# Kernel tuning notes

Measured on AMD Instinct MI355X. Metric: run time of the kernel, lower is better.

The kernel has to match this reference:

```python
import jax, jax.numpy as jnp
import numpy as np

N = 200000      # n_edges (1-simplices)
NNZ = 2000000   # nonzeros per sparse Laplacian
F_IN = 64       # num_edge_feats
F_H = 32        # f_size (hard-coded in FlowSAN)
F_OUT = 8       # output_size
G = 256         # number of graphs in batch
NEG_SLOPE = 0.2 # GAT LeakyReLU slope


def setup_inputs() -> dict:
    key = jax.random.key(0)
    ks = iter(jax.random.split(key, 64))

    def rn(shape, s=0.1):
        return jax.random.normal(next(ks), shape, dtype=jnp.float32) * s

    d = {"x1": jax.random.normal(next(ks), (N, F_IN), dtype=jnp.float32)}
    dims = [(F_IN, F_H), (F_H, F_H), (F_H, F_H), (F_H, F_OUT)]
    for i, (fi, fo) in enumerate(dims, 1):
        d[f"pW{i}"] = rn((fi, fo))                      # SANLayer.p_layer weight (bias=False)
        d[f"uW{i}"] = rn((fi, fo))                      # l_u GAT linear
        d[f"ua_s{i}"] = rn((fo,)); d[f"ua_d{i}"] = rn((fo,))  # l_u GAT attention vec halves
        d[f"dW{i}"] = rn((fi, fo))                      # l_d GAT linear
        d[f"da_s{i}"] = rn((fo,)); d[f"da_d{i}"] = rn((fo,))
    d["l1_idx"] = jax.random.randint(next(ks), (2, NNZ), 0, N, dtype=jnp.int32)
    d["l1_val"] = jax.random.normal(next(ks), (NNZ,), dtype=jnp.float32)
    d["lu_idx"] = jax.random.randint(next(ks), (2, NNZ), 0, N, dtype=jnp.int32)
    d["ld_idx"] = jax.random.randint(next(ks), (2, NNZ), 0, N, dtype=jnp.int32)
    d["batch1"] = jnp.sort(jax.random.randint(next(ks), (N,), 0, G, dtype=jnp.int32))
    return d


def _gat(x, W, a_s, a_d, idx):
    # GAT-style attention over the nonzero pattern of the sparse Laplacian
    h = x @ W                                   # [N, fo]
    row, col = idx[0], idx[1]
    e = jax.nn.leaky_relu(h[row] @ a_s + h[col] @ a_d, NEG_SLOPE)  # [nnz]
    e = e - jax.ops.segment_max(e, row, num_segments=N)[row]       # stable softmax
    w = jnp.exp(e)
    alpha = w / (jax.ops.segment_sum(w, row, num_segments=N)[row] + 1e-16)
    return jax.ops.segment_sum(alpha[:, None] * h[col], row, num_segments=N)


def _san(x, pW, uW, ua_s, ua_d, dW, da_s, da_d, l1_idx, l1_val, lu_idx, ld_idx):
    # p branch: torch.sparse.mm(L1, x @ pW)
    hp = x @ pW
    row, col = l1_idx[0], l1_idx[1]
    hp = jax.ops.segment_sum(l1_val[:, None] * hp[col], row, num_segments=N)
    hu = _gat(x, uW, ua_s, ua_d, lu_idx)
    hd = _gat(x, dW, da_s, da_d, ld_idx)
    return hu + hd + hp


def reference(x1,
              pW1, uW1, ua_s1, ua_d1, dW1, da_s1, da_d1,
              pW2, uW2, ua_s2, ua_d2, dW2, da_s2, da_d2,
              pW3, uW3, ua_s3, ua_d3, dW3, da_s3, da_d3,
              pW4, uW4, ua_s4, ua_d4, dW4, da_s4, da_d4,
              l1_idx, l1_val, lu_idx, ld_idx, batch1):
    layers = [
        (pW1, uW1, ua_s1, ua_d1, dW1, da_s1, da_d1),
        (pW2, uW2, ua_s2, ua_d2, dW2, da_s2, da_d2),
        (pW3, uW3, ua_s3, ua_d3, dW3, da_s3, da_d3),
        (pW4, uW4, ua_s4, ua_d4, dW4, da_s4, da_d4),
    ]
    x = x1
    for p in layers:
        x = jax.nn.relu(_san(x, *p, l1_idx, l1_val, lu_idx, ld_idx))
    # global_mean_pool(|x|, batch1)
    cnt = jax.ops.segment_sum(jnp.ones((N,), jnp.float32), batch1, num_segments=G)
    pooled = jax.ops.segment_sum(jnp.abs(x), batch1, num_segments=G) / jnp.maximum(cnt, 1.0)[:, None]
    return jax.nn.softmax(pooled, axis=1)
```

## Files before the change

### kernel.cpp

```cpp
#include <hip/hip_runtime.h>
#include <cmath>


#define N_    200000
#define NNZ_  2000000
#define G_    256


__global__ __launch_bounds__(256) void hist_k(const int* __restrict__ lu, const int* __restrict__ ld,
                                              const int* __restrict__ l1, int* __restrict__ deg,
                                              int* __restrict__ tick) {
    int i = blockIdx.x * 256 + threadIdx.x;
    if (i >= NNZ_ / 4) return;
    int e = i * 4;
    int4 ru = *reinterpret_cast<const int4*>(lu + e);
    int4 rd = *reinterpret_cast<const int4*>(ld + e);
    int4 rl = *reinterpret_cast<const int4*>(l1 + e);
    int4 t;
    t.x = atomicAdd(&deg[ru.x], 1);
    t.y = atomicAdd(&deg[ru.y], 1);
    t.z = atomicAdd(&deg[ru.z], 1);
    t.w = atomicAdd(&deg[ru.w], 1);
    *reinterpret_cast<int4*>(tick + e) = t;
    t.x = atomicAdd(&deg[N_ + rd.x], 1);
    t.y = atomicAdd(&deg[N_ + rd.y], 1);
    t.z = atomicAdd(&deg[N_ + rd.z], 1);
    t.w = atomicAdd(&deg[N_ + rd.w], 1);
    *reinterpret_cast<int4*>(tick + NNZ_ + e) = t;
    t.x = atomicAdd(&deg[2 * N_ + rl.x], 1);
    t.y = atomicAdd(&deg[2 * N_ + rl.y], 1);
    t.z = atomicAdd(&deg[2 * N_ + rl.z], 1);
    t.w = atomicAdd(&deg[2 * N_ + rl.w], 1);
    *reinterpret_cast<int4*>(tick + 2 * NNZ_ + e) = t;
}

__global__ __launch_bounds__(256) void scan1_k(const int* __restrict__ in, int* __restrict__ out,
                                               int* __restrict__ bsum, int n) {
    __shared__ int lds[256];
    int tid = threadIdx.x;
    int base = blockIdx.x * 1024 + tid * 4;
    int v0 = (base + 0 < n) ? in[base + 0] : 0;
    int v1 = (base + 1 < n) ? in[base + 1] : 0;
    int v2 = (base + 2 < n) ? in[base + 2] : 0;
    int v3 = (base + 3 < n) ? in[base + 3] : 0;
    int s = v0 + v1 + v2 + v3;
    lds[tid] = s;
    __syncthreads();
    for (int off = 1; off < 256; off <<= 1) {
        int t = (tid >= off) ? lds[tid - off] : 0;
        __syncthreads();
        lds[tid] += t;
        __syncthreads();
    }
    int excl = lds[tid] - s;
    if (base + 0 < n) out[base + 0] = excl;
    if (base + 1 < n) out[base + 1] = excl + v0;
    if (base + 2 < n) out[base + 2] = excl + v0 + v1;
    if (base + 3 < n) out[base + 3] = excl + v0 + v1 + v2;
    if (tid == 255) bsum[blockIdx.x] = lds[255];
}

__global__ __launch_bounds__(256) void scan2_k(int* __restrict__ bsum, int nb, int* __restrict__ total_out) {
    __shared__ int lds[256];
    __shared__ int run_s;
    int tid = threadIdx.x;
    if (tid == 0) run_s = 0;
    __syncthreads();
    for (int c0 = 0; c0 < nb; c0 += 256) {
        int i = c0 + tid;
        int s = (i < nb) ? bsum[i] : 0;
        lds[tid] = s;
        __syncthreads();
        for (int off = 1; off < 256; off <<= 1) {
            int t = (tid >= off) ? lds[tid - off] : 0;
            __syncthreads();
            lds[tid] += t;
            __syncthreads();
        }
        int run = run_s;
        if (i < nb) bsum[i] = run + lds[tid] - s;
        __syncthreads();
        if (tid == 0) run_s = run + lds[255];
        __syncthreads();
    }
    if (tid == 0 && total_out) *total_out = run_s;
}

__global__ __launch_bounds__(256) void scan3_k(int* __restrict__ out, const int* __restrict__ bsum, int n) {
    int add = bsum[blockIdx.x];
    int base = blockIdx.x * 1024 + threadIdx.x * 4;
    #pragma unroll
    for (int k = 0; k < 4; ++k)
        if (base + k < n) out[base + k] += add;
}


template <int FI, int FO, int SCB>
__global__ __launch_bounds__(256) void scat_gemm_k(
    const int* __restrict__ lu, const int* __restrict__ ld, const int* __restrict__ l1,
    const float* __restrict__ l1v, const int* __restrict__ rptr, const int* __restrict__ tick,
    int* __restrict__ cols, float* __restrict__ vcsr,
    const float* __restrict__ x,
    const float* __restrict__ uW, const float* __restrict__ uas, const float* __restrict__ uad,
    const float* __restrict__ dW, const float* __restrict__ das, const float* __restrict__ dad,
    const float* __restrict__ pW,
    float* __restrict__ HU, float* __restrict__ HD, float* __restrict__ HP,
    float* __restrict__ ssu, float* __restrict__ sdu,
    float* __restrict__ ssd, float* __restrict__ sdd) {
    if (blockIdx.x < SCB) {
        int i = blockIdx.x * 256 + threadIdx.x;
        if (i >= NNZ_ / 4) return;
        int e = i * 4;
        int4 ru = *reinterpret_cast<const int4*>(lu + e);
        int4 rd = *reinterpret_cast<const int4*>(ld + e);
        int4 rl = *reinterpret_cast<const int4*>(l1 + e);
        int4 cu = *reinterpret_cast<const int4*>(lu + NNZ_ + e);
        int4 cd = *reinterpret_cast<const int4*>(ld + NNZ_ + e);
        int4 cl = *reinterpret_cast<const int4*>(l1 + NNZ_ + e);
        int4 tu = *reinterpret_cast<const int4*>(tick + e);
        int4 td = *reinterpret_cast<const int4*>(tick + NNZ_ + e);
        int4 tl = *reinterpret_cast<const int4*>(tick + 2 * NNZ_ + e);
        float4 v = *reinterpret_cast<const float4*>(l1v + e);
        int pu0 = rptr[ru.x] + tu.x, pu1 = rptr[ru.y] + tu.y;
        int pu2 = rptr[ru.z] + tu.z, pu3 = rptr[ru.w] + tu.w;
        int pd0 = rptr[N_ + rd.x] + td.x, pd1 = rptr[N_ + rd.y] + td.y;
        int pd2 = rptr[N_ + rd.z] + td.z, pd3 = rptr[N_ + rd.w] + td.w;
        int pl0 = rptr[2 * N_ + rl.x] + tl.x, pl1 = rptr[2 * N_ + rl.y] + tl.y;
        int pl2 = rptr[2 * N_ + rl.z] + tl.z, pl3 = rptr[2 * N_ + rl.w] + tl.w;
        __builtin_nontemporal_store(cu.x, &cols[pu0]);
        __builtin_nontemporal_store(cu.y, &cols[pu1]);
        __builtin_nontemporal_store(cu.z, &cols[pu2]);
        __builtin_nontemporal_store(cu.w, &cols[pu3]);
        __builtin_nontemporal_store(cd.x, &cols[pd0]);
        __builtin_nontemporal_store(cd.y, &cols[pd1]);
        __builtin_nontemporal_store(cd.z, &cols[pd2]);
        __builtin_nontemporal_store(cd.w, &cols[pd3]);
        __builtin_nontemporal_store(cl.x, &cols[pl0]);
        __builtin_nontemporal_store(cl.y, &cols[pl1]);
        __builtin_nontemporal_store(cl.z, &cols[pl2]);
        __builtin_nontemporal_store(cl.w, &cols[pl3]);
        __builtin_nontemporal_store(v.x, &vcsr[pl0 - 2 * NNZ_]);
        __builtin_nontemporal_store(v.y, &vcsr[pl1 - 2 * NNZ_]);
        __builtin_nontemporal_store(v.z, &vcsr[pl2 - 2 * NNZ_]);
        __builtin_nontemporal_store(v.w, &vcsr[pl3 - 2 * NNZ_]);
        return;
    }
    int bid = blockIdx.x - SCB;
    constexpr int ROWS = 256 / FO;
    constexpr int XS = FI + 1;
    __shared__ float Wu[FI * FO], Wd[FI * FO], Wp[FI * FO];
    __shared__ float xs[ROWS * XS];
    int tid = threadIdx.x;
    for (int i = tid; i < FI * FO; i += 256) {
        Wu[i] = uW[i];
        Wd[i] = dW[i];
        Wp[i] = pW[i];
    }
    int row0 = bid * ROWS;
    for (int i = tid; i < ROWS * FI; i += 256) {
        int r = i / FI, k = i - r * FI;
        int gr = row0 + r;
        xs[r * XS + k] = (gr < N_) ? x[(size_t)gr * FI + k] : 0.f;
    }
    __syncthreads();
    int r = tid / FO, j = tid - (tid / FO) * FO;
    int grow = row0 + r;
    float au = 0.f, ad = 0.f, ap = 0.f;
    #pragma unroll
    for (int k = 0; k < FI; ++k) {
        float xv = xs[r * XS + k];
        au = fmaf(xv, Wu[k * FO + j], au);
        ad = fmaf(xv, Wd[k * FO + j], ad);
        ap = fmaf(xv, Wp[k * FO + j], ap);
    }
    if (grow < N_) {
        HU[(size_t)grow * FO + j] = au;
        HD[(size_t)grow * FO + j] = ad;
        HP[(size_t)grow * FO + j] = ap;
    }
    float vsu = au * uas[j], vdu = au * uad[j];
    float vsd = ad * das[j], vdd = ad * dad[j];
    #pragma unroll
    for (int m = FO / 2; m >= 1; m >>= 1) {
        vsu += __shfl_xor(vsu, m, FO);
        vdu += __shfl_xor(vdu, m, FO);
        vsd += __shfl_xor(vsd, m, FO);
        vdd += __shfl_xor(vdd, m, FO);
    }
    if (j == 0 && grow < N_) {
        ssu[grow] = vsu; sdu[grow] = vdu;
        ssd[grow] = vsd; sdd[grow] = vdd;
    }
}


template <int FI, int FO>
__global__ __launch_bounds__(256) void gemm3_k(const float* __restrict__ x,
                                               const float* __restrict__ uW, const float* __restrict__ uas,
                                               const float* __restrict__ uad,
                                               const float* __restrict__ dW, const float* __restrict__ das,
                                               const float* __restrict__ dad,
                                               const float* __restrict__ pW,
                                               float* __restrict__ HU, float* __restrict__ HD,
                                               float* __restrict__ HP,
                                               float* __restrict__ ssu, float* __restrict__ sdu,
                                               float* __restrict__ ssd, float* __restrict__ sdd) {
    constexpr int ROWS = 256 / FO;
    constexpr int XS = FI + 1;
    __shared__ float Wu[FI * FO], Wd[FI * FO], Wp[FI * FO];
    __shared__ float xs[ROWS * XS];
    int tid = threadIdx.x;
    for (int i = tid; i < FI * FO; i += 256) {
        Wu[i] = uW[i];
        Wd[i] = dW[i];
        Wp[i] = pW[i];
    }
    int row0 = blockIdx.x * ROWS;
    for (int i = tid; i < ROWS * FI; i += 256) {
        int r = i / FI, k = i - r * FI;
        int gr = row0 + r;
        xs[r * XS + k] = (gr < N_) ? x[(size_t)gr * FI + k] : 0.f;
    }
    __syncthreads();
    int r = tid / FO, j = tid - (tid / FO) * FO;
    int grow = row0 + r;
    float au = 0.f, ad = 0.f, ap = 0.f;
    #pragma unroll
    for (int k = 0; k < FI; ++k) {
        float xv = xs[r * XS + k];
        au = fmaf(xv, Wu[k * FO + j], au);
        ad = fmaf(xv, Wd[k * FO + j], ad);
        ap = fmaf(xv, Wp[k * FO + j], ap);
    }
    if (grow < N_) {
        HU[(size_t)grow * FO + j] = au;
        HD[(size_t)grow * FO + j] = ad;
        HP[(size_t)grow * FO + j] = ap;
    }
    float vsu = au * uas[j], vdu = au * uad[j];
    float vsd = ad * das[j], vdd = ad * dad[j];
    #pragma unroll
    for (int m = FO / 2; m >= 1; m >>= 1) {
        vsu += __shfl_xor(vsu, m, FO);
        vdu += __shfl_xor(vdu, m, FO);
        vsd += __shfl_xor(vsd, m, FO);
        vdd += __shfl_xor(vdd, m, FO);
    }
    if (j == 0 && grow < N_) {
        ssu[grow] = vsu; sdu[grow] = vdu;
        ssd[grow] = vsd; sdd[grow] = vdd;
    }
}


template <int FO, bool GAT>
__device__ __forceinline__ void edge_loop(const int* __restrict__ cols, const float* __restrict__ sdv,
                                          const float* __restrict__ vals, const float* __restrict__ H,
                                          int b, int e, int lane, float s_row, int vbase,
                                          float& ax, float& ay, float& az, float& aw, float& z) {
    for (int p = b; p < e; p += 4) {
        int q1 = p + 1 < e ? p + 1 : e - 1;
        int q2 = p + 2 < e ? p + 2 : e - 1;
        int q3 = p + 3 < e ? p + 3 : e - 1;
        int c0 = cols[p], c1 = cols[q1], c2 = cols[q2], c3 = cols[q3];
        const float4 h0 = *reinterpret_cast<const float4*>(H + (size_t)c0 * FO + lane * 4);
        const float4 h1 = *reinterpret_cast<const float4*>(H + (size_t)c1 * FO + lane * 4);
        const float4 h2 = *reinterpret_cast<const float4*>(H + (size_t)c2 * FO + lane * 4);
        const float4 h3 = *reinterpret_cast<const float4*>(H + (size_t)c3 * FO + lane * 4);
        float w0, w1, w2, w3;
        if constexpr (GAT) {
            float g0 = s_row + sdv[c0];
            float g1 = s_row + sdv[c1];
            float g2 = s_row + sdv[c2];
            float g3 = s_row + sdv[c3];
            g0 = g0 > 0.f ? g0 : 0.2f * g0;
            g1 = g1 > 0.f ? g1 : 0.2f * g1;
            g2 = g2 > 0.f ? g2 : 0.2f * g2;
            g3 = g3 > 0.f ? g3 : 0.2f * g3;
            w0 = __expf(g0);
            w1 = p + 1 < e ? __expf(g1) : 0.f;
            w2 = p + 2 < e ? __expf(g2) : 0.f;
            w3 = p + 3 < e ? __expf(g3) : 0.f;
            z += (w0 + w1) + (w2 + w3);
        } else {
            w0 = vals[p - vbase];
            w1 = p + 1 < e ? vals[q1 - vbase] : 0.f;
            w2 = p + 2 < e ? vals[q2 - vbase] : 0.f;
            w3 = p + 3 < e ? vals[q3 - vbase] : 0.f;
        }
        ax = fmaf(w0, h0.x, ax); ay = fmaf(w0, h0.y, ay);
        az = fmaf(w0, h0.z, az); aw = fmaf(w0, h0.w, aw);
        ax = fmaf(w1, h1.x, ax); ay = fmaf(w1, h1.y, ay);
        az = fmaf(w1, h1.z, az); aw = fmaf(w1, h1.w, aw);
        ax = fmaf(w2, h2.x, ax); ay = fmaf(w2, h2.y, ay);
        az = fmaf(w2, h2.z, az); aw = fmaf(w2, h2.w, aw);
        ax = fmaf(w3, h3.x, ax); ay = fmaf(w3, h3.y, ay);
        az = fmaf(w3, h3.z, az); aw = fmaf(w3, h3.w, aw);
    }
}

template <int FO, int TEAMS>
__global__ __launch_bounds__(256) void gather3_k(const int* __restrict__ rptr, const int* __restrict__ cols,
                                                 const float* __restrict__ vcsr,
                                                 const float* __restrict__ HU, const float* __restrict__ HD,
                                                 const float* __restrict__ HP,
                                                 const float* __restrict__ ssu, const float* __restrict__ sdu,
                                                 const float* __restrict__ ssd, const float* __restrict__ sdd,
                                                 float* __restrict__ xout) {
    constexpr int LPR = FO / 4;
    constexpr int TPR = LPR * TEAMS;
    constexpr int RPB = 256 / TPR;
    int tid = threadIdx.x;
    int lane = tid & (LPR - 1);
    int team = (tid / LPR) & (TEAMS - 1);
    int r = blockIdx.x * RPB + tid / TPR;
    if (r >= N_) return;
    float ox = 0.f, oy = 0.f, oz = 0.f, ow = 0.f;

    auto branch = [&](const float* H, const float* sdv, const float* vals, int base, int vbase,
                      bool gat, float s_row, float& bx, float& by, float& bz, float& bw, float& z) {
        int b0 = rptr[base + r], e0 = rptr[base + r + 1];
        int half = (e0 - b0) >> 1;
        int tb = team == 0 ? b0 : b0 + half;
        int te = team == 0 ? b0 + half : e0;
        if (tb < te) {
            if (gat)
                edge_loop<FO, true>(cols, sdv, nullptr, H, tb, te, lane, s_row, 0, bx, by, bz, bw, z);
            else
                edge_loop<FO, false>(cols, nullptr, vals, H, tb, te, lane, 0.f, vbase, bx, by, bz, bw, z);
        }
        bx += __shfl_xor(bx, LPR, TPR);
        by += __shfl_xor(by, LPR, TPR);
        bz += __shfl_xor(bz, LPR, TPR);
        bw += __shfl_xor(bw, LPR, TPR);
        if (gat) z += __shfl_xor(z, LPR, TPR);
    };

    {
        float ax = 0.f, ay = 0.f, az = 0.f, aw = 0.f, z = 0.f;
        branch(HU, sdu, nullptr, 0, 0, true, ssu[r], ax, ay, az, aw, z);
        float inv = 1.f / (z + 1e-16f);
        ox = ax * inv; oy = ay * inv; oz = az * inv; ow = aw * inv;
    }
    {
        float ax = 0.f, ay = 0.f, az = 0.f, aw = 0.f, z = 0.f;
        branch(HD, sdd, nullptr, N_, 0, true, ssd[r], ax, ay, az, aw, z);
        float inv = 1.f / (z + 1e-16f);
        ox = fmaf(ax, inv, ox); oy = fmaf(ay, inv, oy);
        oz = fmaf(az, inv, oz); ow = fmaf(aw, inv, ow);
    }
    {
        float ax = 0.f, ay = 0.f, az = 0.f, aw = 0.f, z = 0.f;
        branch(HP, nullptr, vcsr, 2 * N_, 2 * NNZ_, false, 0.f, ax, ay, az, aw, z);
        ox += ax; oy += ay; oz += az; ow += aw;
    }
    if (team == 0) {
        ox = fmaxf(ox, 0.f); oy = fmaxf(oy, 0.f);
        oz = fmaxf(oz, 0.f); ow = fmaxf(ow, 0.f);
        *reinterpret_cast<float4*>(xout + (size_t)r * FO + lane * 4) = make_float4(ox, oy, oz, ow);
    }
}


__global__ __launch_bounds__(256) void pool_k(const float* __restrict__ x, const int* __restrict__ batch,
                                              float* __restrict__ out) {
    int g = blockIdx.x;
    __shared__ float part[256];
    __shared__ int sse[2];
    if (threadIdx.x < 2) {
        int target = g + threadIdx.x;
        int lo = 0, hi = N_;
        while (lo < hi) {
            int mid = (lo + hi) >> 1;
            if (batch[mid] < target) lo = mid + 1; else hi = mid;
        }
        sse[threadIdx.x] = lo;
    }
    __syncthreads();
    int s = sse[0], e = sse[1];
    int f = threadIdx.x % 8;
    float acc = 0.f;
    for (int i = s + threadIdx.x / 8; i < e; i += 32) acc += fabsf(x[(size_t)i * 8 + f]);
    part[threadIdx.x] = acc;
    __syncthreads();
    if (threadIdx.x < 8) {
        float t = 0.f;
        #pragma unroll
        for (int k = 0; k < 32; ++k) t += part[k * 8 + f];
        float cnt = (float)(e - s);
        part[f] = t / fmaxf(cnt, 1.0f);
    }
    __syncthreads();
    if (threadIdx.x == 0) {
        float m = part[0];
        for (int j = 1; j < 8; ++j) m = fmaxf(m, part[j]);
        float zs = 0.f;
        float ex[8];
        for (int j = 0; j < 8; ++j) { ex[j] = __expf(part[j] - m); zs += ex[j]; }
        for (int j = 0; j < 8; ++j) out[g * 8 + j] = ex[j] / zs;
    }
}


template <int FI, int FO>
static void run_layer(const float* xin, float* xout, const float* const* W,
                      float* HU, float* HD, float* HP,
                      float* SSU, float* SDU, float* SSD, float* SDD,
                      const int* PTR, const int* COLS, const float* VCSR, hipStream_t stream) {
    constexpr int ROWS = 256 / FO;
    constexpr int RPB = 256 / ((FO / 4) * 2);
    gemm3_k<FI, FO><<<(N_ + ROWS - 1) / ROWS, 256, 0, stream>>>(
        xin, W[1], W[2], W[3], W[4], W[5], W[6], W[0],
        HU, HD, HP, SSU, SDU, SSD, SDD);
    gather3_k<FO, 2><<<(N_ + RPB - 1) / RPB, 256, 0, stream>>>(
        PTR, COLS, VCSR, HU, HD, HP, SSU, SDU, SSD, SDD, xout);
}

extern "C" void kernel_launch(void* const* d_in, const int* in_sizes, int n_in, void* d_out,
                              int out_size, void* d_ws, size_t ws_size, hipStream_t stream) {
    (void)in_sizes; (void)n_in; (void)out_size; (void)ws_size;
    const float* x1     = (const float*)d_in[0];
    const int*   l1_idx = (const int*)d_in[29];
    const float* l1_val = (const float*)d_in[30];
    const int*   lu_idx = (const int*)d_in[31];
    const int*   ld_idx = (const int*)d_in[32];
    const int*   batch1 = (const int*)d_in[33];
    float* out = (float*)d_out;

    char* w = (char*)d_ws;
    size_t off = 0;
    auto alloc = [&](size_t bytes) -> char* {
        char* p = w + off;
        off = (off + bytes + 255) & ~(size_t)255;
        return p;
    };
    float* X    = (float*)alloc((size_t)N_ * 32 * 4);
    float* HU   = (float*)alloc((size_t)N_ * 32 * 4);
    float* HD   = (float*)alloc((size_t)N_ * 32 * 4);
    float* HP   = (float*)alloc((size_t)N_ * 32 * 4);
    float* SSU  = (float*)alloc((size_t)N_ * 4);
    float* SDU  = (float*)alloc((size_t)N_ * 4);
    float* SSD  = (float*)alloc((size_t)N_ * 4);
    float* SDD  = (float*)alloc((size_t)N_ * 4);
    int*   PTR  = (int*)alloc((size_t)(3 * N_ + 1) * 4);
    int*   DEG  = (int*)alloc((size_t)3 * N_ * 4);
    int*   BSUM = (int*)alloc((size_t)1024 * 4);
    int*   TICK = (int*)alloc((size_t)3 * NNZ_ * 4);
    int*   COLS = (int*)alloc((size_t)3 * NNZ_ * 4);
    float* VCSR = (float*)alloc((size_t)NNZ_ * 4);

    const float* W0[7] = {(const float*)d_in[1], (const float*)d_in[2], (const float*)d_in[3],
                          (const float*)d_in[4], (const float*)d_in[5], (const float*)d_in[6],
                          (const float*)d_in[7]};
    const float* W1[7] = {(const float*)d_in[8],  (const float*)d_in[9],  (const float*)d_in[10],
                          (const float*)d_in[11], (const float*)d_in[12], (const float*)d_in[13],
                          (const float*)d_in[14]};
    const float* W2[7] = {(const float*)d_in[15], (const float*)d_in[16], (const float*)d_in[17],
                          (const float*)d_in[18], (const float*)d_in[19], (const float*)d_in[20],
                          (const float*)d_in[21]};
    const float* W3[7] = {(const float*)d_in[22], (const float*)d_in[23], (const float*)d_in[24],
                          (const float*)d_in[25], (const float*)d_in[26], (const float*)d_in[27],
                          (const float*)d_in[28]};

    hipMemsetAsync(DEG, 0, (size_t)3 * N_ * 4, stream);
    constexpr int QBL = (NNZ_ / 4 + 255) / 256;
    hist_k<<<QBL, 256, 0, stream>>>(lu_idx, ld_idx, l1_idx, DEG, TICK);
    int n3 = 3 * N_;
    int nb = (n3 + 1023) / 1024;
    scan1_k<<<nb, 256, 0, stream>>>(DEG, PTR, BSUM, n3);
    scan2_k<<<1, 256, 0, stream>>>(BSUM, nb, PTR + n3);
    scan3_k<<<nb, 256, 0, stream>>>(PTR, BSUM, n3);

    {
        constexpr int ROWS = 256 / 32;
        int gemmb = (N_ + ROWS - 1) / ROWS;
        scat_gemm_k<64, 32, QBL><<<QBL + gemmb, 256, 0, stream>>>(
            lu_idx, ld_idx, l1_idx, l1_val, PTR, TICK, COLS, VCSR,
            x1, W0[1], W0[2], W0[3], W0[4], W0[5], W0[6], W0[0],
            HU, HD, HP, SSU, SDU, SSD, SDD);
    }
    {
        constexpr int RPB = 256 / ((32 / 4) * 2);
        gather3_k<32, 2><<<(N_ + RPB - 1) / RPB, 256, 0, stream>>>(
            PTR, COLS, VCSR, HU, HD, HP, SSU, SDU, SSD, SDD, X);
    }

    run_layer<32, 32>(X, X, W1, HU, HD, HP, SSU, SDU, SSD, SDD, PTR, COLS, VCSR, stream);
    run_layer<32, 32>(X, X, W2, HU, HD, HP, SSU, SDU, SSD, SDD, PTR, COLS, VCSR, stream);
    run_layer<32, 8>(X, X, W3, HU, HD, HP, SSU, SDU, SSD, SDD, PTR, COLS, VCSR, stream);

    pool_k<<<G_, 256, 0, stream>>>(X, batch1, out);
}
```

Measured before the change: 1.544 ms.

## Store projected features in fp16, pack L1 col/val, wave-per-row gather

The per-layer projections HU/HD/HP are now stored as fp16, which halves the bytes fetched by the random neighbour gathers. The L1 column index and value are packed into one int2 per edge, and the u/d column arrays are split into separate buffers. The gather kernel is rewritten to give each row one 64-lane wave: groups of lanes take different edges and each lane reads 8 half features, followed by shuffle reductions. The CSR scatter blocks are interleaved with the first-layer GEMM blocks (every 13th block) so the two kinds of work overlap. The trade-off is reduced precision of the intermediate features and wasted lanes on rows with few edges.

```diff
diff --git a/kernel.cpp b/kernel.cpp
--- a/kernel.cpp
+++ b/kernel.cpp
@@ -1,4 +1,5 @@
 #include <hip/hip_runtime.h>
+#include <hip/hip_fp16.h>
 #include <cmath>
 
 
@@ -99,16 +100,18 @@
 __global__ __launch_bounds__(256) void scat_gemm_k(
     const int* __restrict__ lu, const int* __restrict__ ld, const int* __restrict__ l1,
     const float* __restrict__ l1v, const int* __restrict__ rptr, const int* __restrict__ tick,
-    int* __restrict__ cols, float* __restrict__ vcsr,
+    int* __restrict__ cols_u, int* __restrict__ cols_d, int2* __restrict__ pl,
     const float* __restrict__ x,
     const float* __restrict__ uW, const float* __restrict__ uas, const float* __restrict__ uad,
     const float* __restrict__ dW, const float* __restrict__ das, const float* __restrict__ dad,
     const float* __restrict__ pW,
-    float* __restrict__ HU, float* __restrict__ HD, float* __restrict__ HP,
+    __half* __restrict__ HU, __half* __restrict__ HD, __half* __restrict__ HP,
     float* __restrict__ ssu, float* __restrict__ sdu,
     float* __restrict__ ssd, float* __restrict__ sdd) {
-    if (blockIdx.x < SCB) {
-        int i = blockIdx.x * 256 + threadIdx.x;
+    if (blockIdx.x % 13 == 0) {
+        int sid = blockIdx.x / 13;
+        if (sid >= SCB) return;
+        int i = sid * 256 + threadIdx.x;
         if (i >= NNZ_ / 4) return;
         int e = i * 4;
         int4 ru = *reinterpret_cast<const int4*>(lu + e);
@@ -123,29 +126,29 @@
         float4 v = *reinterpret_cast<const float4*>(l1v + e);
         int pu0 = rptr[ru.x] + tu.x, pu1 = rptr[ru.y] + tu.y;
         int pu2 = rptr[ru.z] + tu.z, pu3 = rptr[ru.w] + tu.w;
-        int pd0 = rptr[N_ + rd.x] + td.x, pd1 = rptr[N_ + rd.y] + td.y;
-        int pd2 = rptr[N_ + rd.z] + td.z, pd3 = rptr[N_ + rd.w] + td.w;
-        int pl0 = rptr[2 * N_ + rl.x] + tl.x, pl1 = rptr[2 * N_ + rl.y] + tl.y;
-        int pl2 = rptr[2 * N_ + rl.z] + tl.z, pl3 = rptr[2 * N_ + rl.w] + tl.w;
-        __builtin_nontemporal_store(cu.x, &cols[pu0]);
-        __builtin_nontemporal_store(cu.y, &cols[pu1]);
-        __builtin_nontemporal_store(cu.z, &cols[pu2]);
-        __builtin_nontemporal_store(cu.w, &cols[pu3]);
-        __builtin_nontemporal_store(cd.x, &cols[pd0]);
-        __builtin_nontemporal_store(cd.y, &cols[pd1]);
-        __builtin_nontemporal_store(cd.z, &cols[pd2]);
-        __builtin_nontemporal_store(cd.w, &cols[pd3]);
-        __builtin_nontemporal_store(cl.x, &cols[pl0]);
-        __builtin_nontemporal_store(cl.y, &cols[pl1]);
-        __builtin_nontemporal_store(cl.z, &cols[pl2]);
-        __builtin_nontemporal_store(cl.w, &cols[pl3]);
-        __builtin_nontemporal_store(v.x, &vcsr[pl0 - 2 * NNZ_]);
-        __builtin_nontemporal_store(v.y, &vcsr[pl1 - 2 * NNZ_]);
-        __builtin_nontemporal_store(v.z, &vcsr[pl2 - 2 * NNZ_]);
-        __builtin_nontemporal_store(v.w, &vcsr[pl3 - 2 * NNZ_]);
+        int pd0 = rptr[N_ + rd.x] + td.x - NNZ_, pd1 = rptr[N_ + rd.y] + td.y - NNZ_;
+        int pd2 = rptr[N_ + rd.z] + td.z - NNZ_, pd3 = rptr[N_ + rd.w] + td.w - NNZ_;
+        int pl0 = rptr[2 * N_ + rl.x] + tl.x - 2 * NNZ_, pl1 = rptr[2 * N_ + rl.y] + tl.y - 2 * NNZ_;
+        int pl2 = rptr[2 * N_ + rl.z] + tl.z - 2 * NNZ_, pl3 = rptr[2 * N_ + rl.w] + tl.w - 2 * NNZ_;
+        __builtin_nontemporal_store(cu.x, &cols_u[pu0]);
+        __builtin_nontemporal_store(cu.y, &cols_u[pu1]);
+        __builtin_nontemporal_store(cu.z, &cols_u[pu2]);
+        __builtin_nontemporal_store(cu.w, &cols_u[pu3]);
+        __builtin_nontemporal_store(cd.x, &cols_d[pd0]);
+        __builtin_nontemporal_store(cd.y, &cols_d[pd1]);
+        __builtin_nontemporal_store(cd.z, &cols_d[pd2]);
+        __builtin_nontemporal_store(cd.w, &cols_d[pd3]);
+        long long q0 = ((long long)__float_as_int(v.x) << 32) | (unsigned)cl.x;
+        long long q1 = ((long long)__float_as_int(v.y) << 32) | (unsigned)cl.y;
+        long long q2 = ((long long)__float_as_int(v.z) << 32) | (unsigned)cl.z;
+        long long q3 = ((long long)__float_as_int(v.w) << 32) | (unsigned)cl.w;
+        __builtin_nontemporal_store(q0, (long long*)&pl[pl0]);
+        __builtin_nontemporal_store(q1, (long long*)&pl[pl1]);
+        __builtin_nontemporal_store(q2, (long long*)&pl[pl2]);
+        __builtin_nontemporal_store(q3, (long long*)&pl[pl3]);
         return;
     }
-    int bid = blockIdx.x - SCB;
+    int gid = blockIdx.x - blockIdx.x / 13 - 1;
     constexpr int ROWS = 256 / FO;
     constexpr int XS = FI + 1;
     __shared__ float Wu[FI * FO], Wd[FI * FO], Wp[FI * FO];
@@ -156,7 +159,7 @@
         Wd[i] = dW[i];
         Wp[i] = pW[i];
     }
-    int row0 = bid * ROWS;
+    int row0 = gid * ROWS;
     for (int i = tid; i < ROWS * FI; i += 256) {
         int r = i / FI, k = i - r * FI;
         int gr = row0 + r;
@@ -174,9 +177,9 @@
         ap = fmaf(xv, Wp[k * FO + j], ap);
     }
     if (grow < N_) {
-        HU[(size_t)grow * FO + j] = au;
-        HD[(size_t)grow * FO + j] = ad;
-        HP[(size_t)grow * FO + j] = ap;
+        HU[(size_t)grow * FO + j] = __float2half(au);
+        HD[(size_t)grow * FO + j] = __float2half(ad);
+        HP[(size_t)grow * FO + j] = __float2half(ap);
     }
     float vsu = au * uas[j], vdu = au * uad[j];
     float vsd = ad * das[j], vdd = ad * dad[j];
@@ -201,8 +204,8 @@
                                                const float* __restrict__ dW, const float* __restrict__ das,
                                                const float* __restrict__ dad,
                                                const float* __restrict__ pW,
-                                               float* __restrict__ HU, float* __restrict__ HD,
-                                               float* __restrict__ HP,
+                                               __half* __restrict__ HU, __half* __restrict__ HD,
+                                               __half* __restrict__ HP,
                                                float* __restrict__ ssu, float* __restrict__ sdu,
                                                float* __restrict__ ssd, float* __restrict__ sdd) {
     constexpr int ROWS = 256 / FO;
@@ -233,9 +236,9 @@
         ap = fmaf(xv, Wp[k * FO + j], ap);
     }
     if (grow < N_) {
-        HU[(size_t)grow * FO + j] = au;
-        HD[(size_t)grow * FO + j] = ad;
-        HP[(size_t)grow * FO + j] = ap;
+        HU[(size_t)grow * FO + j] = __float2half(au);
+        HD[(size_t)grow * FO + j] = __float2half(ad);
+        HP[(size_t)grow * FO + j] = __float2half(ap);
     }
     float vsu = au * uas[j], vdu = au * uad[j];
     float vsd = ad * das[j], vdd = ad * dad[j];
@@ -253,111 +256,102 @@
 }
 
 
-template <int FO, bool GAT>
-__device__ __forceinline__ void edge_loop(const int* __restrict__ cols, const float* __restrict__ sdv,
-                                          const float* __restrict__ vals, const float* __restrict__ H,
-                                          int b, int e, int lane, float s_row, int vbase,
-                                          float& ax, float& ay, float& az, float& aw, float& z) {
-    for (int p = b; p < e; p += 4) {
-        int q1 = p + 1 < e ? p + 1 : e - 1;
-        int q2 = p + 2 < e ? p + 2 : e - 1;
-        int q3 = p + 3 < e ? p + 3 : e - 1;
-        int c0 = cols[p], c1 = cols[q1], c2 = cols[q2], c3 = cols[q3];
-        const float4 h0 = *reinterpret_cast<const float4*>(H + (size_t)c0 * FO + lane * 4);
-        const float4 h1 = *reinterpret_cast<const float4*>(H + (size_t)c1 * FO + lane * 4);
-        const float4 h2 = *reinterpret_cast<const float4*>(H + (size_t)c2 * FO + lane * 4);
-        const float4 h3 = *reinterpret_cast<const float4*>(H + (size_t)c3 * FO + lane * 4);
-        float w0, w1, w2, w3;
-        if constexpr (GAT) {
-            float g0 = s_row + sdv[c0];
-            float g1 = s_row + sdv[c1];
-            float g2 = s_row + sdv[c2];
-            float g3 = s_row + sdv[c3];
-            g0 = g0 > 0.f ? g0 : 0.2f * g0;
-            g1 = g1 > 0.f ? g1 : 0.2f * g1;
-            g2 = g2 > 0.f ? g2 : 0.2f * g2;
-            g3 = g3 > 0.f ? g3 : 0.2f * g3;
-            w0 = __expf(g0);
-            w1 = p + 1 < e ? __expf(g1) : 0.f;
-            w2 = p + 2 < e ? __expf(g2) : 0.f;
-            w3 = p + 3 < e ? __expf(g3) : 0.f;
-            z += (w0 + w1) + (w2 + w3);
-        } else {
-            w0 = vals[p - vbase];
-            w1 = p + 1 < e ? vals[q1 - vbase] : 0.f;
-            w2 = p + 2 < e ? vals[q2 - vbase] : 0.f;
-            w3 = p + 3 < e ? vals[q3 - vbase] : 0.f;
-        }
-        ax = fmaf(w0, h0.x, ax); ay = fmaf(w0, h0.y, ay);
-        az = fmaf(w0, h0.z, az); aw = fmaf(w0, h0.w, aw);
-        ax = fmaf(w1, h1.x, ax); ay = fmaf(w1, h1.y, ay);
-        az = fmaf(w1, h1.z, az); aw = fmaf(w1, h1.w, aw);
-        ax = fmaf(w2, h2.x, ax); ay = fmaf(w2, h2.y, ay);
-        az = fmaf(w2, h2.z, az); aw = fmaf(w2, h2.w, aw);
-        ax = fmaf(w3, h3.x, ax); ay = fmaf(w3, h3.y, ay);
-        az = fmaf(w3, h3.z, az); aw = fmaf(w3, h3.w, aw);
-    }
-}
-
-template <int FO, int TEAMS>
-__global__ __launch_bounds__(256) void gather3_k(const int* __restrict__ rptr, const int* __restrict__ cols,
-                                                 const float* __restrict__ vcsr,
-                                                 const float* __restrict__ HU, const float* __restrict__ HD,
-                                                 const float* __restrict__ HP,
+template <int FO>
+__global__ __launch_bounds__(256) void gather3_k(const int* __restrict__ rptr,
+                                                 const int* __restrict__ cols_u,
+                                                 const int* __restrict__ cols_d,
+                                                 const int2* __restrict__ pl,
+                                                 const __half* __restrict__ HU,
+                                                 const __half* __restrict__ HD,
+                                                 const __half* __restrict__ HP,
                                                  const float* __restrict__ ssu, const float* __restrict__ sdu,
                                                  const float* __restrict__ ssd, const float* __restrict__ sdd,
                                                  float* __restrict__ xout) {
-    constexpr int LPR = FO / 4;
-    constexpr int TPR = LPR * TEAMS;
-    constexpr int RPB = 256 / TPR;
-    int tid = threadIdx.x;
-    int lane = tid & (LPR - 1);
-    int team = (tid / LPR) & (TEAMS - 1);
-    int r = blockIdx.x * RPB + tid / TPR;
+    constexpr int LPR = FO / 8;
+    constexpr int SLOTS = 64 / LPR;
+    int lane = threadIdx.x & 63;
+    int wv = threadIdx.x >> 6;
+    int fs = lane & (LPR - 1);
+    int slot = lane / LPR;
+    int r = blockIdx.x * 4 + wv;
     if (r >= N_) return;
-    float ox = 0.f, oy = 0.f, oz = 0.f, ow = 0.f;
-
-    auto branch = [&](const float* H, const float* sdv, const float* vals, int base, int vbase,
-                      bool gat, float s_row, float& bx, float& by, float& bz, float& bw, float& z) {
-        int b0 = rptr[base + r], e0 = rptr[base + r + 1];
-        int half = (e0 - b0) >> 1;
-        int tb = team == 0 ? b0 : b0 + half;
-        int te = team == 0 ? b0 + half : e0;
-        if (tb < te) {
-            if (gat)
-                edge_loop<FO, true>(cols, sdv, nullptr, H, tb, te, lane, s_row, 0, bx, by, bz, bw, z);
-            else
-                edge_loop<FO, false>(cols, nullptr, vals, H, tb, te, lane, 0.f, vbase, bx, by, bz, bw, z);
+
+    float out[8];
+    #pragma unroll
+    for (int k = 0; k < 8; ++k) out[k] = 0.f;
+
+    #pragma unroll
+    for (int br = 0; br < 2; ++br) {
+        const int* cols = br == 0 ? cols_u : cols_d;
+        const __half* H = br == 0 ? HU : HD;
+        const float* sdv = br == 0 ? sdu : sdd;
+        const float* ssv = br == 0 ? ssu : ssd;
+        int base = br == 0 ? 0 : N_;
+        int boff = br == 0 ? 0 : NNZ_;
+        int b = rptr[base + r] - boff, e = rptr[base + r + 1] - boff;
+        float s_row = ssv[r];
+        float acc[8];
+        #pragma unroll
+        for (int k = 0; k < 8; ++k) acc[k] = 0.f;
+        float z = 0.f;
+        for (int p0 = b; p0 < e; p0 += SLOTS) {
+            int p = p0 + slot;
+            bool valid = p < e;
+            int pc = valid ? p : e - 1;
+            int c = cols[pc];
+            float g = s_row + sdv[c];
+            g = g > 0.f ? g : 0.2f * g;
+            float w = valid ? __expf(g) : 0.f;
+            z += w;
+            const float4 hv = *reinterpret_cast<const float4*>(H + (size_t)c * FO + fs * 8);
+            const __half2* h2 = reinterpret_cast<const __half2*>(&hv);
+            #pragma unroll
+            for (int k = 0; k < 4; ++k) {
+                float2 f = __half22float2(h2[k]);
+                acc[2 * k]     = fmaf(w, f.x, acc[2 * k]);
+                acc[2 * k + 1] = fmaf(w, f.y, acc[2 * k + 1]);
+            }
         }
-        bx += __shfl_xor(bx, LPR, TPR);
-        by += __shfl_xor(by, LPR, TPR);
-        bz += __shfl_xor(bz, LPR, TPR);
-        bw += __shfl_xor(bw, LPR, TPR);
-        if (gat) z += __shfl_xor(z, LPR, TPR);
-    };
+        #pragma unroll
+        for (int m = LPR; m < 64; m <<= 1) z += __shfl_xor(z, m);
+        float inv = 1.f / (z + 1e-16f);
+        #pragma unroll
+        for (int k = 0; k < 8; ++k) out[k] = fmaf(acc[k], inv, out[k]);
+    }
 
     {
-        float ax = 0.f, ay = 0.f, az = 0.f, aw = 0.f, z = 0.f;
-        branch(HU, sdu, nullptr, 0, 0, true, ssu[r], ax, ay, az, aw, z);
-        float inv = 1.f / (z + 1e-16f);
-        ox = ax * inv; oy = ay * inv; oz = az * inv; ow = aw * inv;
-    }
-    {
-        float ax = 0.f, ay = 0.f, az = 0.f, aw = 0.f, z = 0.f;
-        branch(HD, sdd, nullptr, N_, 0, true, ssd[r], ax, ay, az, aw, z);
-        float inv = 1.f / (z + 1e-16f);
-        ox = fmaf(ax, inv, ox); oy = fmaf(ay, inv, oy);
-        oz = fmaf(az, inv, oz); ow = fmaf(aw, inv, ow);
-    }
-    {
-        float ax = 0.f, ay = 0.f, az = 0.f, aw = 0.f, z = 0.f;
-        branch(HP, nullptr, vcsr, 2 * N_, 2 * NNZ_, false, 0.f, ax, ay, az, aw, z);
-        ox += ax; oy += ay; oz += az; ow += aw;
-    }
-    if (team == 0) {
-        ox = fmaxf(ox, 0.f); oy = fmaxf(oy, 0.f);
-        oz = fmaxf(oz, 0.f); ow = fmaxf(ow, 0.f);
-        *reinterpret_cast<float4*>(xout + (size_t)r * FO + lane * 4) = make_float4(ox, oy, oz, ow);
+        int b = rptr[2 * N_ + r] - 2 * NNZ_, e = rptr[2 * N_ + r + 1] - 2 * NNZ_;
+        for (int p0 = b; p0 < e; p0 += SLOTS) {
+            int p = p0 + slot;
+            bool valid = p < e;
+            int pc = valid ? p : e - 1;
+            int2 cv = pl[pc];
+            int c = cv.x;
+            float w = valid ? __int_as_float(cv.y) : 0.f;
+            const float4 hv = *reinterpret_cast<const float4*>(HP + (size_t)c * FO + fs * 8);
+            const __half2* h2 = reinterpret_cast<const __half2*>(&hv);
+            #pragma unroll
+            for (int k = 0; k < 4; ++k) {
+                float2 f = __half22float2(h2[k]);
+                out[2 * k]     = fmaf(w, f.x, out[2 * k]);
+                out[2 * k + 1] = fmaf(w, f.y, out[2 * k + 1]);
+            }
+        }
+    }
+
+    #pragma unroll
+    for (int k = 0; k < 8; ++k) {
+        #pragma unroll
+        for (int m = LPR; m < 64; m <<= 1) out[k] += __shfl_xor(out[k], m);
+    }
+    if (slot == 0) {
+        float4 o0 = make_float4(fmaxf(out[0], 0.f), fmaxf(out[1], 0.f),
+                                fmaxf(out[2], 0.f), fmaxf(out[3], 0.f));
+        float4 o1 = make_float4(fmaxf(out[4], 0.f), fmaxf(out[5], 0.f),
+                                fmaxf(out[6], 0.f), fmaxf(out[7], 0.f));
+        float* op = xout + (size_t)r * FO + fs * 8;
+        *reinterpret_cast<float4*>(op) = o0;
+        *reinterpret_cast<float4*>(op + 4) = o1;
     }
 }
 
@@ -404,16 +398,16 @@
 
 template <int FI, int FO>
 static void run_layer(const float* xin, float* xout, const float* const* W,
-                      float* HU, float* HD, float* HP,
+                      __half* HU, __half* HD, __half* HP,
                       float* SSU, float* SDU, float* SSD, float* SDD,
-                      const int* PTR, const int* COLS, const float* VCSR, hipStream_t stream) {
+                      const int* PTR, const int* CU, const int* CD, const int2* PL,
+                      hipStream_t stream) {
     constexpr int ROWS = 256 / FO;
-    constexpr int RPB = 256 / ((FO / 4) * 2);
     gemm3_k<FI, FO><<<(N_ + ROWS - 1) / ROWS, 256, 0, stream>>>(
         xin, W[1], W[2], W[3], W[4], W[5], W[6], W[0],
         HU, HD, HP, SSU, SDU, SSD, SDD);
-    gather3_k<FO, 2><<<(N_ + RPB - 1) / RPB, 256, 0, stream>>>(
-        PTR, COLS, VCSR, HU, HD, HP, SSU, SDU, SSD, SDD, xout);
+    gather3_k<FO><<<(N_ + 3) / 4, 256, 0, stream>>>(
+        PTR, CU, CD, PL, HU, HD, HP, SSU, SDU, SSD, SDD, xout);
 }
 
 extern "C" void kernel_launch(void* const* d_in, const int* in_sizes, int n_in, void* d_out,
@@ -434,20 +428,21 @@
         off = (off + bytes + 255) & ~(size_t)255;
         return p;
     };
-    float* X    = (float*)alloc((size_t)N_ * 32 * 4);
-    float* HU   = (float*)alloc((size_t)N_ * 32 * 4);
-    float* HD   = (float*)alloc((size_t)N_ * 32 * 4);
-    float* HP   = (float*)alloc((size_t)N_ * 32 * 4);
-    float* SSU  = (float*)alloc((size_t)N_ * 4);
-    float* SDU  = (float*)alloc((size_t)N_ * 4);
-    float* SSD  = (float*)alloc((size_t)N_ * 4);
-    float* SDD  = (float*)alloc((size_t)N_ * 4);
-    int*   PTR  = (int*)alloc((size_t)(3 * N_ + 1) * 4);
-    int*   DEG  = (int*)alloc((size_t)3 * N_ * 4);
-    int*   BSUM = (int*)alloc((size_t)1024 * 4);
-    int*   TICK = (int*)alloc((size_t)3 * NNZ_ * 4);
-    int*   COLS = (int*)alloc((size_t)3 * NNZ_ * 4);
-    float* VCSR = (float*)alloc((size_t)NNZ_ * 4);
+    float*  X    = (float*)alloc((size_t)N_ * 32 * 4);
+    __half* HU   = (__half*)alloc((size_t)N_ * 32 * 2);
+    __half* HD   = (__half*)alloc((size_t)N_ * 32 * 2);
+    __half* HP   = (__half*)alloc((size_t)N_ * 32 * 2);
+    float*  SSU  = (float*)alloc((size_t)N_ * 4);
+    float*  SDU  = (float*)alloc((size_t)N_ * 4);
+    float*  SSD  = (float*)alloc((size_t)N_ * 4);
+    float*  SDD  = (float*)alloc((size_t)N_ * 4);
+    int*    PTR  = (int*)alloc((size_t)(3 * N_ + 1) * 4);
+    int*    DEG  = (int*)alloc((size_t)3 * N_ * 4);
+    int*    BSUM = (int*)alloc((size_t)1024 * 4);
+    int*    TICK = (int*)alloc((size_t)3 * NNZ_ * 4);
+    int*    CU   = (int*)alloc((size_t)NNZ_ * 4);
+    int*    CD   = (int*)alloc((size_t)NNZ_ * 4);
+    int2*   PL   = (int2*)alloc((size_t)NNZ_ * 8);
 
     const float* W0[7] = {(const float*)d_in[1], (const float*)d_in[2], (const float*)d_in[3],
                           (const float*)d_in[4], (const float*)d_in[5], (const float*)d_in[6],
@@ -472,22 +467,18 @@
     scan3_k<<<nb, 256, 0, stream>>>(PTR, BSUM, n3);
 
     {
-        constexpr int ROWS = 256 / 32;
-        int gemmb = (N_ + ROWS - 1) / ROWS;
-        scat_gemm_k<64, 32, QBL><<<QBL + gemmb, 256, 0, stream>>>(
-            lu_idx, ld_idx, l1_idx, l1_val, PTR, TICK, COLS, VCSR,
+        constexpr int T = 27100;
+        scat_gemm_k<64, 32, QBL><<<T, 256, 0, stream>>>(
+            lu_idx, ld_idx, l1_idx, l1_val, PTR, TICK, CU, CD, PL,
             x1, W0[1], W0[2], W0[3], W0[4], W0[5], W0[6], W0[0],
             HU, HD, HP, SSU, SDU, SSD, SDD);
     }
-    {
-        constexpr int RPB = 256 / ((32 / 4) * 2);
-        gather3_k<32, 2><<<(N_ + RPB - 1) / RPB, 256, 0, stream>>>(
-            PTR, COLS, VCSR, HU, HD, HP, SSU, SDU, SSD, SDD, X);
-    }
-
-    run_layer<32, 32>(X, X, W1, HU, HD, HP, SSU, SDU, SSD, SDD, PTR, COLS, VCSR, stream);
-    run_layer<32, 32>(X, X, W2, HU, HD, HP, SSU, SDU, SSD, SDD, PTR, COLS, VCSR, stream);
-    run_layer<32, 8>(X, X, W3, HU, HD, HP, SSU, SDU, SSD, SDD, PTR, COLS, VCSR, stream);
+    gather3_k<32><<<(N_ + 3) / 4, 256, 0, stream>>>(
+        PTR, CU, CD, PL, HU, HD, HP, SSU, SDU, SSD, SDD, X);
+
+    run_layer<32, 32>(X, X, W1, HU, HD, HP, SSU, SDU, SSD, SDD, PTR, CU, CD, PL, stream);
+    run_layer<32, 32>(X, X, W2, HU, HD, HP, SSU, SDU, SSD, SDD, PTR, CU, CD, PL, stream);
+    run_layer<32, 8>(X, X, W3, HU, HD, HP, SSU, SDU, SSD, SDD, PTR, CU, CD, PL, stream);
 
     pool_k<<<G_, 256, 0, stream>>>(X, batch1, out);
 }
```

Result: faster. 1.474 ms (-4.5%).
